# Kernel optimization log

Hardware: AMD Instinct MI355X
Metric: run time of the kernel (lower is better)

The kernel has to match this reference:

```python
import jax, jax.numpy as jnp
import numpy as np

HSIZE = 128
E = 640000


def _init_linear(key, fan_in, fan_out):
    # torch nn.Linear default init: U(-1/sqrt(fan_in), 1/sqrt(fan_in))
    kw, kb = jax.random.split(key)
    bound = 1.0 / np.sqrt(fan_in)
    W = jax.random.uniform(kw, (fan_in, fan_out), jnp.float32, -bound, bound)
    b = jax.random.uniform(kb, (fan_out,), jnp.float32, -bound, bound)
    return W, b


def setup_inputs() -> dict:
    key = jax.random.key(0)
    ks = jax.random.split(key, 6)
    hself = jax.random.normal(ks[0], (E, HSIZE), jnp.float32)
    hother = jax.random.normal(ks[1], (E, HSIZE), jnp.float32)
    Wm1, bm1 = _init_linear(ks[2], 2 * HSIZE, HSIZE)
    Wm2, bm2 = _init_linear(ks[3], HSIZE, HSIZE)
    Wu1, bu1 = _init_linear(ks[4], 2 * HSIZE, HSIZE)
    Wu2, bu2 = _init_linear(ks[5], HSIZE, HSIZE)
    return {"hself": hself, "hother": hother,
            "Wm1": Wm1, "bm1": bm1, "Wm2": Wm2, "bm2": bm2,
            "Wu1": Wu1, "bu1": bu1, "Wu2": Wu2, "bu2": bu2}


def _mlp2(a, b, W1, b1, W2, b2):
    # concat([a, b], -1) @ W1 done without materializing the concat
    h = a @ W1[:HSIZE] + b @ W1[HSIZE:] + b1
    h = jax.nn.relu(h)
    return h @ W2 + b2


def reference(hself, hother, Wm1, bm1, Wm2, bm2, Wu1, bu1, Wu2, bu2):
    # msg: Linear(2h,h) -> ReLU -> Linear(h,h) on cat([hself, hother])
    msg = _mlp2(hself, hother, Wm1, bm1, Wm2, bm2)
    # upd: Linear(2h,h) -> ReLU -> Linear(h,h) on cat([hself, msg])
    out = _mlp2(hself, msg, Wu1, bu1, Wu2, bu2)
    return out
```

## Files before the change

### kernel.cpp

```cpp
#include <hip/hip_runtime.h>

typedef __bf16 bf16_t;
typedef __bf16 bf16x8 __attribute__((ext_vector_type(8)));
typedef float f32x4 __attribute__((ext_vector_type(4)));

#define MFMA(a, b, c) __builtin_amdgcn_mfma_f32_16x16x32_bf16((a), (b), (c), 0, 0, 0)

#define E_ROWS 640000
#define BM 256

static __device__ __forceinline__ bf16x8 cvt8(float4 a, float4 b) {
  bf16x8 r;
  r[0] = (bf16_t)a.x; r[1] = (bf16_t)a.y; r[2] = (bf16_t)a.z; r[3] = (bf16_t)a.w;
  r[4] = (bf16_t)b.x; r[5] = (bf16_t)b.y; r[6] = (bf16_t)b.z; r[7] = (bf16_t)b.w;
  return r;
}

static __device__ __forceinline__ unsigned int pk2(float a, float b) {
  unsigned short ua = __builtin_bit_cast(unsigned short, (bf16_t)a);
  unsigned short ub = __builtin_bit_cast(unsigned short, (bf16_t)b);
  return ((unsigned int)ub << 16) | ua;
}

static __device__ __forceinline__ void gload_lds16(const void* g, void* l) {
  __builtin_amdgcn_global_load_lds(
      (const __attribute__((address_space(1))) unsigned int*)g,
      (__attribute__((address_space(3))) unsigned int*)l, 16, 0, 0);
}

__global__ __launch_bounds__(256) void prep_weights(
    const float* __restrict__ Wm1, const float* __restrict__ Wm2,
    const float* __restrict__ Wu1, const float* __restrict__ Wu2,
    bf16_t* __restrict__ wt) {
  int c = blockIdx.x * 256 + threadIdx.x;
  if (c >= 12288) return;
  int lane = c & 63, f = c >> 6;
  const float* W; int base;
  if (f < 64)       { W = Wm1; base = 0;   }
  else if (f < 96)  { W = Wm2; base = 64;  }
  else if (f < 160) { W = Wu1; base = 96;  }
  else              { W = Wu2; base = 160; }
  int fl = f - base;
  int ks = fl >> 3, nb = fl & 7;
  int k0 = 32 * ks + 8 * (lane >> 4);
  int n  = 16 * nb + (lane & 15);
  bf16x8 v;
  #pragma unroll
  for (int j = 0; j < 8; ++j) v[j] = (bf16_t)W[(size_t)(k0 + j) * 128 + n];
  ((bf16x8*)wt)[c] = v;
}

#define STAGE96(tc0) { \
  _Pragma("unroll") \
  for (int i_ = 0; i_ < 12; ++i_) \
    gload_lds16((const char*)wt + ((size_t)((tc0) + i_ * 512 + tid)) * 16, \
                smem + (i_ * 512 + tid) * 16); }

#define LDW8(s, base, fl0) \
  s##0 = *(const bf16x8*)((base) + ((fl0) + 0) * 1024 + lane * 16); \
  s##1 = *(const bf16x8*)((base) + ((fl0) + 1) * 1024 + lane * 16); \
  s##2 = *(const bf16x8*)((base) + ((fl0) + 2) * 1024 + lane * 16); \
  s##3 = *(const bf16x8*)((base) + ((fl0) + 3) * 1024 + lane * 16); \
  s##4 = *(const bf16x8*)((base) + ((fl0) + 4) * 1024 + lane * 16); \
  s##5 = *(const bf16x8*)((base) + ((fl0) + 5) * 1024 + lane * 16); \
  s##6 = *(const bf16x8*)((base) + ((fl0) + 6) * 1024 + lane * 16); \
  s##7 = *(const bf16x8*)((base) + ((fl0) + 7) * 1024 + lane * 16);

#define ROUND(s, x0, x1) \
  acc00 = MFMA(s##0, x0, acc00); acc10 = MFMA(s##0, x1, acc10); \
  acc01 = MFMA(s##1, x0, acc01); acc11 = MFMA(s##1, x1, acc11); \
  acc02 = MFMA(s##2, x0, acc02); acc12 = MFMA(s##2, x1, acc12); \
  acc03 = MFMA(s##3, x0, acc03); acc13 = MFMA(s##3, x1, acc13); \
  acc04 = MFMA(s##4, x0, acc04); acc14 = MFMA(s##4, x1, acc14); \
  acc05 = MFMA(s##5, x0, acc05); acc15 = MFMA(s##5, x1, acc15); \
  acc06 = MFMA(s##6, x0, acc06); acc16 = MFMA(s##6, x1, acc16); \
  acc07 = MFMA(s##7, x0, acc07); acc17 = MFMA(s##7, x1, acc17);

#define ACCINIT(bp) { const float* bp_ = (bp) + g * 4; float4 q; \
  q = *(const float4*)(bp_ +   0); acc00 = (f32x4){q.x,q.y,q.z,q.w}; acc10 = acc00; \
  q = *(const float4*)(bp_ +  16); acc01 = (f32x4){q.x,q.y,q.z,q.w}; acc11 = acc01; \
  q = *(const float4*)(bp_ +  32); acc02 = (f32x4){q.x,q.y,q.z,q.w}; acc12 = acc02; \
  q = *(const float4*)(bp_ +  48); acc03 = (f32x4){q.x,q.y,q.z,q.w}; acc13 = acc03; \
  q = *(const float4*)(bp_ +  64); acc04 = (f32x4){q.x,q.y,q.z,q.w}; acc14 = acc04; \
  q = *(const float4*)(bp_ +  80); acc05 = (f32x4){q.x,q.y,q.z,q.w}; acc15 = acc05; \
  q = *(const float4*)(bp_ +  96); acc06 = (f32x4){q.x,q.y,q.z,q.w}; acc16 = acc06; \
  q = *(const float4*)(bp_ + 112); acc07 = (f32x4){q.x,q.y,q.z,q.w}; acc17 = acc07; }

#define RPK_H(av, nb, R) { \
  f32x4 v = av; \
  float e0 = v[0], e1 = v[1], e2 = v[2], e3 = v[3]; \
  if (R) { e0 = fmaxf(e0, 0.f); e1 = fmaxf(e1, 0.f); \
           e2 = fmaxf(e2, 0.f); e3 = fmaxf(e3, 0.f); } \
  uint2 w; w.x = pk2(e0, e1); w.y = pk2(e2, e3); \
  int dl = c + 16 * (2 * ((nb) & 1) + (g >> 1)); \
  *(uint2*)(myrep + (((nb) >> 1) * 64 + dl) * 16 + (g & 1) * 8) = w; }

#define WAITLDS asm volatile("s_waitcnt lgkmcnt(0)" ::: "memory");
#define VMCNT0  asm volatile("s_waitcnt vmcnt(0)" ::: "memory");
#define VMCNT32 asm volatile("s_waitcnt vmcnt(32)" ::: "memory");
#define SBAR    __builtin_amdgcn_sched_barrier(0);

#define REPACK(R) \
  RPK_H(acc00, 0, R) RPK_H(acc01, 1, R) RPK_H(acc02, 2, R) RPK_H(acc03, 3, R) \
  RPK_H(acc04, 4, R) RPK_H(acc05, 5, R) RPK_H(acc06, 6, R) RPK_H(acc07, 7, R) \
  WAITLDS \
  x00 = *(const bf16x8*)(myrep + (0 * 64 + lane) * 16); \
  x01 = *(const bf16x8*)(myrep + (1 * 64 + lane) * 16); \
  x02 = *(const bf16x8*)(myrep + (2 * 64 + lane) * 16); \
  x03 = *(const bf16x8*)(myrep + (3 * 64 + lane) * 16); \
  WAITLDS \
  RPK_H(acc10, 0, R) RPK_H(acc11, 1, R) RPK_H(acc12, 2, R) RPK_H(acc13, 3, R) \
  RPK_H(acc14, 4, R) RPK_H(acc15, 5, R) RPK_H(acc16, 6, R) RPK_H(acc17, 7, R) \
  WAITLDS \
  x10 = *(const bf16x8*)(myrep + (0 * 64 + lane) * 16); \
  x11 = *(const bf16x8*)(myrep + (1 * 64 + lane) * 16); \
  x12 = *(const bf16x8*)(myrep + (2 * 64 + lane) * 16); \
  x13 = *(const bf16x8*)(myrep + (3 * 64 + lane) * 16); \
  WAITLDS

#define LOADX(d0, d1, basep, kk) { \
  float4 a0 = *(const float4*)((basep) + r0 + (kk) * 32); \
  float4 a1 = *(const float4*)((basep) + r0 + (kk) * 32 + 4); \
  float4 b0 = *(const float4*)((basep) + r1 + (kk) * 32); \
  float4 b1 = *(const float4*)((basep) + r1 + (kk) * 32 + 4); \
  d0 = cvt8(a0, a1); d1 = cvt8(b0, b1); }

#define ST(av, mt, nb) { f32x4 v = av; \
  *(float4*)(out + (rowbase + (mt) * 16 + c) * 128 + (nb) * 16 + g * 4) = \
      (float4){v[0], v[1], v[2], v[3]}; }

__global__ __launch_bounds__(512) void fused_mp(
    const float* __restrict__ hself, const float* __restrict__ hother,
    const bf16_t* __restrict__ wt,
    const float* __restrict__ bm1, const float* __restrict__ bm2,
    const float* __restrict__ bu1, const float* __restrict__ bu2,
    float* __restrict__ out) {
  __shared__ char smem[131072];

  const int tid = threadIdx.x;
  const int lane = tid & 63;
  const int wave = tid >> 6;
  const int c = lane & 15;
  const int g = lane >> 4;

  char* W1 = smem;
  char* W2 = smem + 65536;
  char* myrep = smem + 98304 + wave * 4096;

  const size_t rowbase = (size_t)blockIdx.x * BM + wave * 32;
  const size_t r0 = (rowbase + c) * 128 + g * 8;
  const size_t r1 = (rowbase + 16 + c) * 128 + g * 8;

  bf16x8 hs00, hs01, hs02, hs03, hs10, hs11, hs12, hs13;
  bf16x8 x00, x01, x02, x03, x10, x11, x12, x13;
  STAGE96(0)
  SBAR
  LOADX(hs00, hs10, hself, 0)
  LOADX(hs01, hs11, hself, 1)
  LOADX(hs02, hs12, hself, 2)
  LOADX(hs03, hs13, hself, 3)
  LOADX(x00, x10, hother, 0)
  LOADX(x01, x11, hother, 1)
  LOADX(x02, x12, hother, 2)
  LOADX(x03, x13, hother, 3)
  SBAR
  VMCNT32
  __syncthreads();

  f32x4 acc00, acc01, acc02, acc03, acc04, acc05, acc06, acc07;
  f32x4 acc10, acc11, acc12, acc13, acc14, acc15, acc16, acc17;
  bf16x8 wa0, wa1, wa2, wa3, wa4, wa5, wa6, wa7;

  ACCINIT(bm1)
  LDW8(wa, W1, 0)   ROUND(wa, hs00, hs10)
  LDW8(wa, W1, 8)   ROUND(wa, hs01, hs11)
  LDW8(wa, W1, 16)  ROUND(wa, hs02, hs12)
  LDW8(wa, W1, 24)  ROUND(wa, hs03, hs13)
  LDW8(wa, W1, 32)  ROUND(wa, x00, x10)
  LDW8(wa, W1, 40)  ROUND(wa, x01, x11)
  LDW8(wa, W1, 48)  ROUND(wa, x02, x12)
  LDW8(wa, W1, 56)  ROUND(wa, x03, x13)

  REPACK(true)

  ACCINIT(bm2)
  LDW8(wa, W2, 0)   ROUND(wa, x00, x10)
  LDW8(wa, W2, 8)   ROUND(wa, x01, x11)
  LDW8(wa, W2, 16)  ROUND(wa, x02, x12)
  LDW8(wa, W2, 24)  ROUND(wa, x03, x13)

  REPACK(false)

  __syncthreads();
  STAGE96(6144)
  VMCNT0
  __syncthreads();

  ACCINIT(bu1)
  LDW8(wa, W1, 0)   ROUND(wa, hs00, hs10)
  LDW8(wa, W1, 8)   ROUND(wa, hs01, hs11)
  LDW8(wa, W1, 16)  ROUND(wa, hs02, hs12)
  LDW8(wa, W1, 24)  ROUND(wa, hs03, hs13)
  LDW8(wa, W1, 32)  ROUND(wa, x00, x10)
  LDW8(wa, W1, 40)  ROUND(wa, x01, x11)
  LDW8(wa, W1, 48)  ROUND(wa, x02, x12)
  LDW8(wa, W1, 56)  ROUND(wa, x03, x13)

  REPACK(true)

  ACCINIT(bu2)
  LDW8(wa, W2, 0)   ROUND(wa, x00, x10)
  LDW8(wa, W2, 8)   ROUND(wa, x01, x11)
  LDW8(wa, W2, 16)  ROUND(wa, x02, x12)
  LDW8(wa, W2, 24)  ROUND(wa, x03, x13)

  ST(acc00, 0, 0) ST(acc01, 0, 1) ST(acc02, 0, 2) ST(acc03, 0, 3)
  ST(acc04, 0, 4) ST(acc05, 0, 5) ST(acc06, 0, 6) ST(acc07, 0, 7)
  ST(acc10, 1, 0) ST(acc11, 1, 1) ST(acc12, 1, 2) ST(acc13, 1, 3)
  ST(acc14, 1, 4) ST(acc15, 1, 5) ST(acc16, 1, 6) ST(acc17, 1, 7)
}

extern "C" void kernel_launch(void* const* d_in, const int* in_sizes, int n_in,
                              void* d_out, int out_size, void* d_ws, size_t ws_size,
                              hipStream_t stream) {
  const float* hself  = (const float*)d_in[0];
  const float* hother = (const float*)d_in[1];
  const float* Wm1 = (const float*)d_in[2];
  const float* bm1 = (const float*)d_in[3];
  const float* Wm2 = (const float*)d_in[4];
  const float* bm2 = (const float*)d_in[5];
  const float* Wu1 = (const float*)d_in[6];
  const float* bu1 = (const float*)d_in[7];
  const float* Wu2 = (const float*)d_in[8];
  const float* bu2 = (const float*)d_in[9];
  float* out = (float*)d_out;
  bf16_t* wt = (bf16_t*)d_ws;

  prep_weights<<<48, 256, 0, stream>>>(Wm1, Wm2, Wu1, Wu2, wt);
  fused_mp<<<E_ROWS / BM, 512, 0, stream>>>(hself, hother, wt,
                                            bm1, bm2, bu1, bu2, out);
}
```

Baseline: 290.3 us.

## Overlap second-stage weight staging with compute using larger LDS buffer

LDS grows from 128 KB to 160 KB so the first half of Wu1 can be staged up front with Wm1/Wm2. The rest of the update weights (Wu1 bottom half and Wu2) is then loaded into the freed Wm1 region asynchronously while the message MLP's second layer and the first half of the update layer run. This hides weight-load latency that the old code exposed behind a full barrier between the two MLPs. The cost is more shared memory per block, which may limit occupancy, and a more intricate buffer reuse schedule.

```diff
diff --git a/kernel.cpp b/kernel.cpp
--- a/kernel.cpp
+++ b/kernel.cpp
@@ -50,10 +50,15 @@
   ((bf16x8*)wt)[c] = v;
 }
 
-#define STAGE96(tc0) { \
+#define STAGE128_B0 { \
   _Pragma("unroll") \
-  for (int i_ = 0; i_ < 12; ++i_) \
-    gload_lds16((const char*)wt + ((size_t)((tc0) + i_ * 512 + tid)) * 16, \
+  for (int i_ = 0; i_ < 16; ++i_) \
+    gload_lds16((const char*)wt + ((size_t)(i_ * 512 + tid)) * 16, \
+                smem + (i_ * 512 + tid) * 16); }
+#define STAGE64_B1 { \
+  _Pragma("unroll") \
+  for (int i_ = 0; i_ < 8; ++i_) \
+    gload_lds16((const char*)wt + ((size_t)(8192 + i_ * 512 + tid)) * 16, \
                 smem + (i_ * 512 + tid) * 16); }
 
 #define LDW8(s, base, fl0) \
@@ -135,7 +140,7 @@
     const float* __restrict__ bm1, const float* __restrict__ bm2,
     const float* __restrict__ bu1, const float* __restrict__ bu2,
     float* __restrict__ out) {
-  __shared__ char smem[131072];
+  __shared__ char smem[163840];
 
   const int tid = threadIdx.x;
   const int lane = tid & 63;
@@ -145,7 +150,8 @@
 
   char* W1 = smem;
   char* W2 = smem + 65536;
-  char* myrep = smem + 98304 + wave * 4096;
+  char* W3 = smem + 98304;
+  char* myrep = smem + 131072 + wave * 4096;
 
   const size_t rowbase = (size_t)blockIdx.x * BM + wave * 32;
   const size_t r0 = (rowbase + c) * 128 + g * 8;
@@ -153,7 +159,7 @@
 
   bf16x8 hs00, hs01, hs02, hs03, hs10, hs11, hs12, hs13;
   bf16x8 x00, x01, x02, x03, x10, x11, x12, x13;
-  STAGE96(0)
+  STAGE128_B0
   SBAR
   LOADX(hs00, hs10, hself, 0)
   LOADX(hs01, hs11, hself, 1)
@@ -180,6 +186,9 @@
   LDW8(wa, W1, 40)  ROUND(wa, x01, x11)
   LDW8(wa, W1, 48)  ROUND(wa, x02, x12)
   LDW8(wa, W1, 56)  ROUND(wa, x03, x13)
+  __syncthreads();
+
+  STAGE64_B1
 
   REPACK(true)
 
@@ -191,28 +200,25 @@
 
   REPACK(false)
 
-  __syncthreads();
-  STAGE96(6144)
+  ACCINIT(bu1)
+  LDW8(wa, W3, 0)   ROUND(wa, hs00, hs10)
+  LDW8(wa, W3, 8)   ROUND(wa, hs01, hs11)
+  LDW8(wa, W3, 16)  ROUND(wa, hs02, hs12)
+  LDW8(wa, W3, 24)  ROUND(wa, hs03, hs13)
   VMCNT0
   __syncthreads();
-
-  ACCINIT(bu1)
-  LDW8(wa, W1, 0)   ROUND(wa, hs00, hs10)
-  LDW8(wa, W1, 8)   ROUND(wa, hs01, hs11)
-  LDW8(wa, W1, 16)  ROUND(wa, hs02, hs12)
-  LDW8(wa, W1, 24)  ROUND(wa, hs03, hs13)
-  LDW8(wa, W1, 32)  ROUND(wa, x00, x10)
-  LDW8(wa, W1, 40)  ROUND(wa, x01, x11)
-  LDW8(wa, W1, 48)  ROUND(wa, x02, x12)
-  LDW8(wa, W1, 56)  ROUND(wa, x03, x13)
+  LDW8(wa, W1, 0)   ROUND(wa, x00, x10)
+  LDW8(wa, W1, 8)   ROUND(wa, x01, x11)
+  LDW8(wa, W1, 16)  ROUND(wa, x02, x12)
+  LDW8(wa, W1, 24)  ROUND(wa, x03, x13)
 
   REPACK(true)
 
   ACCINIT(bu2)
-  LDW8(wa, W2, 0)   ROUND(wa, x00, x10)
-  LDW8(wa, W2, 8)   ROUND(wa, x01, x11)
-  LDW8(wa, W2, 16)  ROUND(wa, x02, x12)
-  LDW8(wa, W2, 24)  ROUND(wa, x03, x13)
+  LDW8(wa, W1 + 32768, 0)   ROUND(wa, x00, x10)
+  LDW8(wa, W1 + 32768, 8)   ROUND(wa, x01, x11)
+  LDW8(wa, W1 + 32768, 16)  ROUND(wa, x02, x12)
+  LDW8(wa, W1 + 32768, 24)  ROUND(wa, x03, x13)
 
   ST(acc00, 0, 0) ST(acc01, 0, 1) ST(acc02, 0, 2) ST(acc03, 0, 3)
   ST(acc04, 0, 4) ST(acc05, 0, 5) ST(acc06, 0, 6) ST(acc07, 0, 7)
```

Result: slower. 534.8 us (+84.3%).
